# Kernel optimization log

Measured on AMD Instinct MI355X. Metric: run time of the kernel, lower is better.

The kernel has to match this reference:

```python
import jax, jax.numpy as jnp
import numpy as np
import math

B, S, D, H = 2, 2048, 1024, 32
HD = D // H  # head_dim = 32
NEG = -1e9


def setup_inputs() -> dict:
    key = jax.random.key(0)
    ks = jax.random.split(key, 6)
    x = jax.random.normal(ks[0], (B, S, D), dtype=jnp.float32)
    # additive causal mask: 0 on/below diagonal, -1e9 above
    causal = jnp.tril(jnp.ones((S, S), dtype=bool))
    mask = jnp.where(causal, 0.0, NEG).astype(jnp.float32)[None, None]
    # SSMax-style per-query-position log-length scale
    section_log_len = jnp.log(jnp.arange(1, S + 1, dtype=jnp.float32) + 1.0).reshape(1, 1, S, 1)
    sc = 1.0 / math.sqrt(D)
    wq = jax.random.normal(ks[1], (D, D), dtype=jnp.float32) * sc
    wk = jax.random.normal(ks[2], (D, D), dtype=jnp.float32) * sc
    wv = jax.random.normal(ks[3], (D, D), dtype=jnp.float32) * sc
    wo = jax.random.normal(ks[4], (D, D), dtype=jnp.float32) * sc
    seq_scale = jnp.ones((1, H, 1, 1), dtype=jnp.float32)
    return {"x": x, "mask": mask, "section_log_len": section_log_len,
            "wq": wq, "wk": wk, "wv": wv, "wo": wo, "seq_scale": seq_scale}


def reference(x, mask, section_log_len, wq, wk, wv, wo, seq_scale):
    bsz, seqlen, dim = x.shape
    # projections (torch Linear: y = x @ W.T); split heads -> [b, h, s, hd]
    q = (x @ wq.T).reshape(bsz, seqlen, H, HD).transpose(0, 2, 1, 3)
    k = (x @ wk.T).reshape(bsz, seqlen, H, HD).transpose(0, 2, 1, 3)
    v = (x @ wv.T).reshape(bsz, seqlen, H, HD).transpose(0, 2, 1, 3)
    # n_kv_heads == n_heads, so repeat_kv is identity
    scores = jnp.einsum('bhqd,bhkd->bhqk', q, k) / math.sqrt(HD)
    scores = scores * (section_log_len * seq_scale)  # SSMax per-head learned scale
    scores = scores + mask
    probs = jax.nn.softmax(scores.astype(jnp.float32), axis=-1).astype(q.dtype)
    out = jnp.einsum('bhqk,bhkd->bhqd', probs, v)
    out = out.transpose(0, 2, 1, 3).reshape(bsz, seqlen, dim)
    return out @ wo.T
```

## Files before the change

kernel.cpp:

```cpp
#include <hip/hip_runtime.h>
#include <hip/hip_bf16.h>

typedef __bf16 bf16_t;
typedef bf16_t bf16x8 __attribute__((ext_vector_type(8)));
typedef float f32x4 __attribute__((ext_vector_type(4)));

#define NB 2
#define SEQ 2048
#define DIM 1024
#define NH 32
#define HDIM 32

#define LDP 72

static __device__ __forceinline__ f32x4 mfma16(bf16x8 a, bf16x8 b, f32x4 c) {
    return __builtin_amdgcn_mfma_f32_16x16x32_bf16(a, b, c, 0, 0, 0);
}

static __device__ __forceinline__ float fexp2(float x) {
    float r;
    asm("v_exp_f32 %0, %1" : "=v"(r) : "v"(x));
    return r;
}

static __device__ __forceinline__ void load_lds16(const bf16_t* g, bf16_t* l) {
    __builtin_amdgcn_global_load_lds(
        (const __attribute__((address_space(1))) void*)(g),
        (__attribute__((address_space(3))) void*)(l), 16, 0, 0);
}

__global__ __launch_bounds__(256)
void cvt_f32_bf16(const float* __restrict__ s0, bf16_t* __restrict__ d0, int n0,
                  const float* __restrict__ s1, bf16_t* __restrict__ d1, int n1,
                  const float* __restrict__ s2, bf16_t* __restrict__ d2, int n2,
                  const float* __restrict__ s3, bf16_t* __restrict__ d3, int n3,
                  const float* __restrict__ s4, bf16_t* __restrict__ d4, int n4) {
    const int stride = gridDim.x * blockDim.x;
    const int tid = blockIdx.x * blockDim.x + threadIdx.x;
    const float* src[5] = {s0, s1, s2, s3, s4};
    bf16_t* dst[5] = {d0, d1, d2, d3, d4};
    const int n[5] = {n0, n1, n2, n3, n4};
#pragma unroll
    for (int r = 0; r < 5; r++) {
        const int nv = n[r] >> 2;
        for (int i = tid; i < nv; i += stride) {
            float4 v = ((const float4*)src[r])[i];
            bf16_t o[4] = {(bf16_t)v.x, (bf16_t)v.y, (bf16_t)v.z, (bf16_t)v.w};
            *(uint2*)(dst[r] + i * 4) = *(const uint2*)o;
        }
    }
}

template <int EPI, int BM>
__global__ __launch_bounds__(256)
void gemm_pipe(const bf16_t* __restrict__ A, const bf16_t* __restrict__ W,
               float* __restrict__ Cf, bf16_t* __restrict__ qb,
               bf16_t* __restrict__ kb, bf16_t* __restrict__ vtb,
               const float* __restrict__ slen, const float* __restrict__ ss) {
    constexpr int MI = BM / 32;
    constexpr int ABUF = BM * 32;
    __shared__ alignas(16) bf16_t As[3 * ABUF];
    __shared__ alignas(16) bf16_t Bs[3 * 4096];
    const int t = threadIdx.x;
    const int lane = t & 63, wave = t >> 6;
    const int lane16 = lane & 15, quad = lane >> 4;
    const int wm = (wave >> 1) * (BM / 2), wn = (wave & 1) * 64;
    const int id = blockIdx.x;
    int m0, n0g;
    if (EPI == 1) {
        const int xcd = id & 7, slot = id >> 3;
        m0 = (xcd + 8 * (slot & 3)) * 128;
        n0g = (slot >> 2) * 128;
    } else {
        const int xcd = id & 7, slot = id >> 3;
        m0 = (xcd + 8 * (slot & 7)) * 64;
        n0g = (slot >> 3) * 128;
    }
    const int tr = t >> 2;
    const int tc = ((t & 3) ^ ((tr >> 1) & 3)) * 8;
    const bf16_t* ga = A + (m0 + tr) * DIM + tc;
    const bf16_t* gb = W + (n0g + tr) * DIM + tc;
    const int rq = (quad ^ ((lane16 >> 1) & 3)) * 8;
    const bool vseg = (EPI == 1) && (n0g >= 2048);

    f32x4 acc[MI][4];
#pragma unroll
    for (int i = 0; i < MI; i++)
#pragma unroll
        for (int j = 0; j < 4; j++) acc[i][j] = f32x4{0.f, 0.f, 0.f, 0.f};

    auto stage = [&](int k0, int buf) {
        bf16_t* a_dst = As + buf * ABUF + (t & 192) * 8;
        bf16_t* b_dst = Bs + buf * 4096 + (t & 192) * 8;
        load_lds16(ga + k0, a_dst);
        if (BM == 128) load_lds16(ga + 64 * DIM + k0, a_dst + 2048);
        load_lds16(gb + k0, b_dst);
        load_lds16(gb + 64 * DIM + k0, b_dst + 2048);
    };
    auto compute = [&](int buf) {
        bf16x8 af[MI], bfr[4];
#pragma unroll
        for (int mi = 0; mi < MI; mi++)
            af[mi] = *(const bf16x8*)(As + buf * ABUF +
                                      (wm + mi * 16 + lane16) * 32 + rq);
#pragma unroll
        for (int ni = 0; ni < 4; ni++)
            bfr[ni] = *(const bf16x8*)(Bs + buf * 4096 +
                                       (wn + ni * 16 + lane16) * 32 + rq);
        if (vseg) {
#pragma unroll
            for (int mi = 0; mi < MI; mi++)
#pragma unroll
                for (int ni = 0; ni < 4; ni++)
                    acc[mi][ni] = mfma16(bfr[ni], af[mi], acc[mi][ni]);
        } else {
#pragma unroll
            for (int mi = 0; mi < MI; mi++)
#pragma unroll
                for (int ni = 0; ni < 4; ni++)
                    acc[mi][ni] = mfma16(af[mi], bfr[ni], acc[mi][ni]);
        }
    };

    stage(0, 0);
    stage(32, 1);
#pragma unroll
    for (int k0 = 0; k0 < DIM; k0 += 32) {
        const int it = k0 >> 5;
        const int cur = it % 3;
        if (k0 + 64 < DIM) {
            stage(k0 + 64, (it + 2) % 3);
            if (BM == 128)
                asm volatile("s_waitcnt vmcnt(8)" ::: "memory");
            else
                asm volatile("s_waitcnt vmcnt(6)" ::: "memory");
        } else if (k0 + 32 < DIM) {
            if (BM == 128)
                asm volatile("s_waitcnt vmcnt(4)" ::: "memory");
            else
                asm volatile("s_waitcnt vmcnt(3)" ::: "memory");
        } else {
            asm volatile("s_waitcnt vmcnt(0)" ::: "memory");
        }
        asm volatile("s_barrier" ::: "memory");
        compute(cur);
        if (k0 + 32 < DIM) {
            asm volatile("s_waitcnt lgkmcnt(0)" ::: "memory");
            asm volatile("s_barrier" ::: "memory");
        }
    }

    if (EPI == 0) {
#pragma unroll
        for (int mi = 0; mi < MI; mi++)
#pragma unroll
            for (int ni = 0; ni < 4; ni++)
#pragma unroll
                for (int r = 0; r < 4; r++) {
                    int row = m0 + wm + mi * 16 + quad * 4 + r;
                    int col = n0g + wn + ni * 16 + lane16;
                    Cf[row * DIM + col] = acc[mi][ni][r];
                }
    } else if (!vseg) {
        const bool isq = (n0g < 1024);
        bf16_t* dst = isq ? qb : kb;
        const int nb = n0g & 1023;
#pragma unroll
        for (int mi = 0; mi < MI; mi++)
#pragma unroll
            for (int ni = 0; ni < 4; ni++) {
                const int h = ((nb + wn) >> 5) + (ni >> 1);
                const float hscale =
                    isq ? ss[h] * (0.17677669529663687f * 1.4426950408889634f)
                        : 0.f;
#pragma unroll
                for (int r = 0; r < 4; r++) {
                    int m = m0 + wm + mi * 16 + quad * 4 + r;
                    int nl = nb + wn + ni * 16 + lane16;
                    int b = m >> 11, s = m & (SEQ - 1);
                    int d = nl & 31;
                    float v = acc[mi][ni][r];
                    if (isq) v *= slen[s] * hscale;
                    dst[(((b * NH + h) << 11) + s) * 32 + d] = (bf16_t)v;
                }
            }
    } else {
        const int nb = n0g & 1023;
#pragma unroll
        for (int mi = 0; mi < MI; mi++)
#pragma unroll
            for (int ni = 0; ni < 4; ni++)
#pragma unroll
                for (int r = 0; r < 4; r++) {
                    int nl = nb + wn + ni * 16 + quad * 4 + r;
                    int m = m0 + wm + mi * 16 + lane16;
                    int b = m >> 11, s = m & (SEQ - 1);
                    int h = nl >> 5, d = nl & 31;
                    vtb[(((b * NH + h) << 5) + d) * SEQ + s] = (bf16_t)acc[mi][ni][r];
                }
    }
}

__global__ __launch_bounds__(256, 4)
void attn_fwd(const bf16_t* __restrict__ q, const bf16_t* __restrict__ k,
              const bf16_t* __restrict__ vt, bf16_t* __restrict__ out) {
    __shared__ alignas(16) bf16_t pscr[4][2][32 * LDP];
    const int t = threadIdx.x;
    const int lane = t & 63, wave = t >> 6;
    const int lane16 = lane & 15, quad = lane >> 4;
    const int gw = blockIdx.x * 4 + wave;
    const int idx = gw & 63;
    const int qt = (idx & 1) ? (63 - (idx >> 1)) : (idx >> 1);
    const int h = (gw >> 6) & (NH - 1);
    const int b = gw >> 11;
    const int q0 = qt * 32;
    const bf16_t* qh = q + (b * NH + h) * SEQ * HDIM;
    const bf16_t* kh = k + (b * NH + h) * SEQ * HDIM;
    const bf16_t* vth = vt + (b * NH + h) * HDIM * SEQ;

    bf16_t* wb0 = pscr[wave][0] + quad * 4 * LDP + 4 * lane16;
    bf16_t* wb1 = pscr[wave][1] + quad * 4 * LDP + 4 * lane16;
    const bf16_t* rb0 = pscr[wave][0] + lane16 * LDP + quad * 8;
    const bf16_t* rb1 = pscr[wave][1] + lane16 * LDP + quad * 8;

    bf16x8 qf[2];
    qf[0] = *(const bf16x8*)(qh + (q0 + lane16) * HDIM + quad * 8);
    qf[1] = *(const bf16x8*)(qh + (q0 + 16 + lane16) * HDIM + quad * 8);

    bf16x8 ones;
#pragma unroll
    for (int j = 0; j < 8; j++) ones[j] = (bf16_t)1.0f;

    f32x4 o[2][2], ol[2];
#pragma unroll
    for (int mi = 0; mi < 2; mi++) {
        ol[mi] = f32x4{0.f, 0.f, 0.f, 0.f};
#pragma unroll
        for (int ni = 0; ni < 2; ni++) o[mi][ni] = f32x4{0.f, 0.f, 0.f, 0.f};
    }

    const bf16_t* kptr = kh + (4 * lane16) * HDIM + quad * 8;
    const bf16_t* vpa = vth + lane16 * SEQ + quad * 8;
    const bf16_t* vpb = vth + (16 + lane16) * SEQ + quad * 8;

    const f32x4 zz = f32x4{0.f, 0.f, 0.f, 0.f};
    bf16x8 kc[4], vc[4], pf[2][2];

    const int nb64 = (qt >> 1) + 1;

    auto qkexp = [&](int hh, bf16_t* wb, int kv, bool domask) {
        f32x4 sc[2][2];
        __builtin_amdgcn_s_setprio(1);
#pragma unroll
        for (int mi = 0; mi < 2; mi++)
#pragma unroll
            for (int j = 0; j < 2; j++)
                sc[mi][j] = mfma16(qf[mi], kc[2 * hh + j], zz);
        __builtin_amdgcn_s_setprio(0);
#pragma unroll
        for (int mi = 0; mi < 2; mi++)
#pragma unroll
            for (int r = 0; r < 4; r++) {
                float p0 = fexp2(sc[mi][0][r]);
                float p1 = fexp2(sc[mi][1][r]);
                if (domask) {
                    const int rowg = q0 + mi * 16 + quad * 4 + r;
                    if (kv + 4 * lane16 + 2 * hh > rowg) p0 = 0.f;
                    if (kv + 4 * lane16 + 2 * hh + 1 > rowg) p1 = 0.f;
                }
                bf16_t pb[2] = {(bf16_t)p0, (bf16_t)p1};
                *(unsigned int*)(wb + (mi * 16 + r) * LDP + 2 * hh) =
                    *(const unsigned int*)pb;
            }
    };
    auto ldk = [&]() {
#pragma unroll
        for (int tt = 0; tt < 4; tt++) kc[tt] = *(const bf16x8*)(kptr + tt * HDIM);
        kptr += 64 * HDIM;
    };
    auto ldv = [&](int kv) {
        vc[0] = *(const bf16x8*)(vpa + kv);
        vc[1] = *(const bf16x8*)(vpa + kv + 32);
        vc[2] = *(const bf16x8*)(vpb + kv);
        vc[3] = *(const bf16x8*)(vpb + kv + 32);
    };
    auto ldp = [&](const bf16_t* rb) {
#pragma unroll
        for (int mi = 0; mi < 2; mi++) {
            pf[mi][0] = *(const bf16x8*)(rb + mi * 16 * LDP);
            pf[mi][1] = *(const bf16x8*)(rb + mi * 16 * LDP + 32);
        }
    };
    auto pv = [&]() {
        __builtin_amdgcn_s_setprio(1);
#pragma unroll
        for (int mi = 0; mi < 2; mi++) {
#pragma unroll
            for (int ni = 0; ni < 2; ni++) {
                o[mi][ni] = mfma16(pf[mi][0], vc[2 * ni], o[mi][ni]);
                o[mi][ni] = mfma16(pf[mi][1], vc[2 * ni + 1], o[mi][ni]);
            }
            ol[mi] = mfma16(pf[mi][0], ones, ol[mi]);
            ol[mi] = mfma16(pf[mi][1], ones, ol[mi]);
        }
        __builtin_amdgcn_s_setprio(0);
    };

    ldk();
    ldv(0);
    {
        const bool m0only = (nb64 == 1);
        qkexp(0, wb0, 0, m0only);
        bf16x8 ksave[4];
        qkexp(1, wb0, 0, m0only);
        (void)ksave;
        ldk();
    }

    for (int i = 1; i < nb64 - 1; i++) {
        const int kv = i << 6;
        bf16_t* wb = (i & 1) ? wb1 : wb0;
        const bf16_t* rb = (i & 1) ? rb0 : rb1;
        ldp(rb);
        pv();
        ldv(kv);
        qkexp(0, wb, kv, false);
        qkexp(1, wb, kv, false);
        ldk();
    }

    if (nb64 > 1) {
        const int i = nb64 - 1;
        const int kv = i << 6;
        bf16_t* wb = (i & 1) ? wb1 : wb0;
        const bf16_t* rb = (i & 1) ? rb0 : rb1;
        ldp(rb);
        pv();
        ldv(kv);
        qkexp(0, wb, kv, true);
        qkexp(1, wb, kv, true);
    }

    ldp(((nb64 - 1) & 1) ? rb1 : rb0);
    pv();

#pragma unroll
    for (int mi = 0; mi < 2; mi++)
#pragma unroll
        for (int r = 0; r < 4; r++) {
            float inv = 1.0f / ol[mi][r];
            int qi = q0 + mi * 16 + quad * 4 + r;
            bf16_t* ob = out + (b * SEQ + qi) * DIM + h * HDIM;
            ob[lane16] = (bf16_t)(o[mi][0][r] * inv);
            ob[16 + lane16] = (bf16_t)(o[mi][1][r] * inv);
        }
}

extern "C" void kernel_launch(void* const* d_in, const int* in_sizes, int n_in,
                              void* d_out, int out_size, void* d_ws, size_t ws_size,
                              hipStream_t stream) {
    const float* x = (const float*)d_in[0];
    const float* slen = (const float*)d_in[2];
    const float* wq = (const float*)d_in[3];
    const float* wk = (const float*)d_in[4];
    const float* wv = (const float*)d_in[5];
    const float* wo = (const float*)d_in[6];
    const float* ss = (const float*)d_in[7];

    const size_t ELEMS = (size_t)NB * SEQ * DIM;
    const size_t WELEMS = (size_t)DIM * DIM;
    bf16_t* xb = (bf16_t*)d_ws;
    bf16_t* abuf = xb;
    bf16_t* wqkvb = xb + ELEMS;
    bf16_t* wob = wqkvb + 3 * WELEMS;
    bf16_t* qbuf = wob + WELEMS;
    bf16_t* vtbuf = qbuf + ELEMS;
    bf16_t* kbuf = (bf16_t*)d_out;

    dim3 blk(256);
    cvt_f32_bf16<<<dim3(1024), blk, 0, stream>>>(
        x, xb, (int)ELEMS, wq, wqkvb, (int)WELEMS, wk, wqkvb + WELEMS,
        (int)WELEMS, wv, wqkvb + 2 * WELEMS, (int)WELEMS, wo, wob, (int)WELEMS);

    gemm_pipe<1, 128><<<dim3(768), blk, 0, stream>>>(
        xb, wqkvb, nullptr, qbuf, kbuf, vtbuf, slen, ss);
    attn_fwd<<<dim3(NB * NH * (SEQ / 32) / 4), blk, 0, stream>>>(
        qbuf, kbuf, vtbuf, abuf);
    gemm_pipe<0, 64><<<dim3(512), blk, 0, stream>>>(
        abuf, wob, (float*)d_out, nullptr, nullptr, nullptr, nullptr, nullptr);
}
```

Baseline: 210.6 us.

## Balance causal attention by pairing short and long query tiles with split-KV combine

Each block now holds two wave pairs. In each pair, one wave processes a short query tile and then the first part of a long tile's KV range. The other wave processes the rest of that long tile, and partial outputs and row sums are added through LDS before the store. This gives every wave an equal count of 64-wide KV blocks and removes the causal load imbalance. In exchange, the P-scratch double buffering and the K prefetch across iterations are dropped, which adds an LDS combine and a block barrier and may expose more memory latency.

```diff
diff --git a/kernel.cpp b/kernel.cpp
--- a/kernel.cpp
+++ b/kernel.cpp
@@ -204,156 +204,166 @@
 __global__ __launch_bounds__(256, 4)
 void attn_fwd(const bf16_t* __restrict__ q, const bf16_t* __restrict__ k,
               const bf16_t* __restrict__ vt, bf16_t* __restrict__ out) {
-    __shared__ alignas(16) bf16_t pscr[4][2][32 * LDP];
+    __shared__ alignas(16) bf16_t pscr[4][32 * LDP];
+    __shared__ float comb[2][64][25];
     const int t = threadIdx.x;
     const int lane = t & 63, wave = t >> 6;
     const int lane16 = lane & 15, quad = lane >> 4;
-    const int gw = blockIdx.x * 4 + wave;
-    const int idx = gw & 63;
-    const int qt = (idx & 1) ? (63 - (idx >> 1)) : (idx >> 1);
-    const int h = (gw >> 6) & (NH - 1);
-    const int b = gw >> 11;
-    const int q0 = qt * 32;
+    const int bh = blockIdx.x & 63;
+    const int g = blockIdx.x >> 6;
+    const int pairi = wave >> 1;
+    const int role = wave & 1;
+    const int tb = g * 2 + pairi;
+    const int qtA = tb, qtB = 63 - tb;
+    const int naA = (qtA >> 1) + 1;
+    const int nbB = (qtB >> 1) + 1;
+    const int split = 16 - naA;
+    const int h = bh & (NH - 1);
+    const int b = bh >> 5;
     const bf16_t* qh = q + (b * NH + h) * SEQ * HDIM;
     const bf16_t* kh = k + (b * NH + h) * SEQ * HDIM;
     const bf16_t* vth = vt + (b * NH + h) * HDIM * SEQ;
 
-    bf16_t* wb0 = pscr[wave][0] + quad * 4 * LDP + 4 * lane16;
-    bf16_t* wb1 = pscr[wave][1] + quad * 4 * LDP + 4 * lane16;
-    const bf16_t* rb0 = pscr[wave][0] + lane16 * LDP + quad * 8;
-    const bf16_t* rb1 = pscr[wave][1] + lane16 * LDP + quad * 8;
-
-    bf16x8 qf[2];
-    qf[0] = *(const bf16x8*)(qh + (q0 + lane16) * HDIM + quad * 8);
-    qf[1] = *(const bf16x8*)(qh + (q0 + 16 + lane16) * HDIM + quad * 8);
-
-    bf16x8 ones;
-#pragma unroll
-    for (int j = 0; j < 8; j++) ones[j] = (bf16_t)1.0f;
-
-    f32x4 o[2][2], ol[2];
-#pragma unroll
-    for (int mi = 0; mi < 2; mi++) {
-        ol[mi] = f32x4{0.f, 0.f, 0.f, 0.f};
-#pragma unroll
-        for (int ni = 0; ni < 2; ni++) o[mi][ni] = f32x4{0.f, 0.f, 0.f, 0.f};
-    }
-
-    const bf16_t* kptr = kh + (4 * lane16) * HDIM + quad * 8;
+    bf16_t* wb = pscr[wave] + quad * 4 * LDP + 4 * lane16;
+    const bf16_t* rb = pscr[wave] + lane16 * LDP + quad * 8;
+
+    const bf16_t* kp0 = kh + (4 * lane16) * HDIM + quad * 8;
     const bf16_t* vpa = vth + lane16 * SEQ + quad * 8;
     const bf16_t* vpb = vth + (16 + lane16) * SEQ + quad * 8;
 
+    bf16x8 ones;
+#pragma unroll
+    for (int j = 0; j < 8; j++) ones[j] = (bf16_t)1.0f;
+
     const f32x4 zz = f32x4{0.f, 0.f, 0.f, 0.f};
-    bf16x8 kc[4], vc[4], pf[2][2];
-
-    const int nb64 = (qt >> 1) + 1;
-
-    auto qkexp = [&](int hh, bf16_t* wb, int kv, bool domask) {
-        f32x4 sc[2][2];
-        __builtin_amdgcn_s_setprio(1);
+    bf16x8 qf[2];
+    f32x4 o[2][2], ol[2];
+
+    auto zeroacc = [&]() {
+#pragma unroll
+        for (int mi = 0; mi < 2; mi++) {
+            ol[mi] = f32x4{0.f, 0.f, 0.f, 0.f};
+#pragma unroll
+            for (int ni = 0; ni < 2; ni++) o[mi][ni] = f32x4{0.f, 0.f, 0.f, 0.f};
+        }
+    };
+    auto loadQ = [&](int q0) {
+        qf[0] = *(const bf16x8*)(qh + (q0 + lane16) * HDIM + quad * 8);
+        qf[1] = *(const bf16x8*)(qh + (q0 + 16 + lane16) * HDIM + quad * 8);
+    };
+    auto doRange = [&](int q0, int lo, int hi, bool maskLast) {
+        for (int blk = lo; blk < hi; blk++) {
+            const int kv = blk << 6;
+            const bool dm = maskLast && (blk == hi - 1);
+            bf16x8 kc[4], vc[4], pf[2][2];
+            const bf16_t* ks = kp0 + blk * (64 * HDIM);
+#pragma unroll
+            for (int tt = 0; tt < 4; tt++)
+                kc[tt] = *(const bf16x8*)(ks + tt * HDIM);
+            vc[0] = *(const bf16x8*)(vpa + kv);
+            vc[1] = *(const bf16x8*)(vpa + kv + 32);
+            vc[2] = *(const bf16x8*)(vpb + kv);
+            vc[3] = *(const bf16x8*)(vpb + kv + 32);
+#pragma unroll
+            for (int hh = 0; hh < 2; hh++) {
+                f32x4 sc[2][2];
+                __builtin_amdgcn_s_setprio(1);
+#pragma unroll
+                for (int mi = 0; mi < 2; mi++)
+#pragma unroll
+                    for (int j = 0; j < 2; j++)
+                        sc[mi][j] = mfma16(qf[mi], kc[2 * hh + j], zz);
+                __builtin_amdgcn_s_setprio(0);
+#pragma unroll
+                for (int mi = 0; mi < 2; mi++)
+#pragma unroll
+                    for (int r = 0; r < 4; r++) {
+                        float p0 = fexp2(sc[mi][0][r]);
+                        float p1 = fexp2(sc[mi][1][r]);
+                        if (dm) {
+                            const int rowg = q0 + mi * 16 + quad * 4 + r;
+                            if (kv + 4 * lane16 + 2 * hh > rowg) p0 = 0.f;
+                            if (kv + 4 * lane16 + 2 * hh + 1 > rowg) p1 = 0.f;
+                        }
+                        bf16_t pb[2] = {(bf16_t)p0, (bf16_t)p1};
+                        *(unsigned int*)(wb + (mi * 16 + r) * LDP + 2 * hh) =
+                            *(const unsigned int*)pb;
+                    }
+            }
+            asm volatile("s_waitcnt lgkmcnt(0)" ::: "memory");
+#pragma unroll
+            for (int mi = 0; mi < 2; mi++) {
+                pf[mi][0] = *(const bf16x8*)(rb + mi * 16 * LDP);
+                pf[mi][1] = *(const bf16x8*)(rb + mi * 16 * LDP + 32);
+            }
+            __builtin_amdgcn_s_setprio(1);
+#pragma unroll
+            for (int mi = 0; mi < 2; mi++) {
+#pragma unroll
+                for (int ni = 0; ni < 2; ni++) {
+                    o[mi][ni] = mfma16(pf[mi][0], vc[2 * ni], o[mi][ni]);
+                    o[mi][ni] = mfma16(pf[mi][1], vc[2 * ni + 1], o[mi][ni]);
+                }
+                ol[mi] = mfma16(pf[mi][0], ones, ol[mi]);
+                ol[mi] = mfma16(pf[mi][1], ones, ol[mi]);
+            }
+            __builtin_amdgcn_s_setprio(0);
+        }
+    };
+    auto storeTile = [&](int q0) {
 #pragma unroll
         for (int mi = 0; mi < 2; mi++)
 #pragma unroll
-            for (int j = 0; j < 2; j++)
-                sc[mi][j] = mfma16(qf[mi], kc[2 * hh + j], zz);
-        __builtin_amdgcn_s_setprio(0);
+            for (int r = 0; r < 4; r++) {
+                float inv = 1.0f / ol[mi][r];
+                int qi = q0 + mi * 16 + quad * 4 + r;
+                bf16_t* ob = out + (b * SEQ + qi) * DIM + h * HDIM;
+                ob[lane16] = (bf16_t)(o[mi][0][r] * inv);
+                ob[16 + lane16] = (bf16_t)(o[mi][1][r] * inv);
+            }
+    };
+
+    if (role == 0) {
+        zeroacc();
+        loadQ(qtA * 32);
+        doRange(qtA * 32, 0, naA, true);
+        storeTile(qtA * 32);
+        zeroacc();
+        loadQ(qtB * 32);
+        doRange(qtB * 32, 0, split, false);
+        float* cl = &comb[pairi][lane][0];
 #pragma unroll
         for (int mi = 0; mi < 2; mi++)
 #pragma unroll
-            for (int r = 0; r < 4; r++) {
-                float p0 = fexp2(sc[mi][0][r]);
-                float p1 = fexp2(sc[mi][1][r]);
-                if (domask) {
-                    const int rowg = q0 + mi * 16 + quad * 4 + r;
-                    if (kv + 4 * lane16 + 2 * hh > rowg) p0 = 0.f;
-                    if (kv + 4 * lane16 + 2 * hh + 1 > rowg) p1 = 0.f;
-                }
-                bf16_t pb[2] = {(bf16_t)p0, (bf16_t)p1};
-                *(unsigned int*)(wb + (mi * 16 + r) * LDP + 2 * hh) =
-                    *(const unsigned int*)pb;
-            }
-    };
-    auto ldk = [&]() {
-#pragma unroll
-        for (int tt = 0; tt < 4; tt++) kc[tt] = *(const bf16x8*)(kptr + tt * HDIM);
-        kptr += 64 * HDIM;
-    };
-    auto ldv = [&](int kv) {
-        vc[0] = *(const bf16x8*)(vpa + kv);
-        vc[1] = *(const bf16x8*)(vpa + kv + 32);
-        vc[2] = *(const bf16x8*)(vpb + kv);
-        vc[3] = *(const bf16x8*)(vpb + kv + 32);
-    };
-    auto ldp = [&](const bf16_t* rb) {
-#pragma unroll
-        for (int mi = 0; mi < 2; mi++) {
-            pf[mi][0] = *(const bf16x8*)(rb + mi * 16 * LDP);
-            pf[mi][1] = *(const bf16x8*)(rb + mi * 16 * LDP + 32);
-        }
-    };
-    auto pv = [&]() {
-        __builtin_amdgcn_s_setprio(1);
-#pragma unroll
-        for (int mi = 0; mi < 2; mi++) {
-#pragma unroll
-            for (int ni = 0; ni < 2; ni++) {
-                o[mi][ni] = mfma16(pf[mi][0], vc[2 * ni], o[mi][ni]);
-                o[mi][ni] = mfma16(pf[mi][1], vc[2 * ni + 1], o[mi][ni]);
-            }
-            ol[mi] = mfma16(pf[mi][0], ones, ol[mi]);
-            ol[mi] = mfma16(pf[mi][1], ones, ol[mi]);
-        }
-        __builtin_amdgcn_s_setprio(0);
-    };
-
-    ldk();
-    ldv(0);
-    {
-        const bool m0only = (nb64 == 1);
-        qkexp(0, wb0, 0, m0only);
-        bf16x8 ksave[4];
-        qkexp(1, wb0, 0, m0only);
-        (void)ksave;
-        ldk();
-    }
-
-    for (int i = 1; i < nb64 - 1; i++) {
-        const int kv = i << 6;
-        bf16_t* wb = (i & 1) ? wb1 : wb0;
-        const bf16_t* rb = (i & 1) ? rb0 : rb1;
-        ldp(rb);
-        pv();
-        ldv(kv);
-        qkexp(0, wb, kv, false);
-        qkexp(1, wb, kv, false);
-        ldk();
-    }
-
-    if (nb64 > 1) {
-        const int i = nb64 - 1;
-        const int kv = i << 6;
-        bf16_t* wb = (i & 1) ? wb1 : wb0;
-        const bf16_t* rb = (i & 1) ? rb0 : rb1;
-        ldp(rb);
-        pv();
-        ldv(kv);
-        qkexp(0, wb, kv, true);
-        qkexp(1, wb, kv, true);
-    }
-
-    ldp(((nb64 - 1) & 1) ? rb1 : rb0);
-    pv();
-
-#pragma unroll
-    for (int mi = 0; mi < 2; mi++)
-#pragma unroll
-        for (int r = 0; r < 4; r++) {
-            float inv = 1.0f / ol[mi][r];
-            int qi = q0 + mi * 16 + quad * 4 + r;
-            bf16_t* ob = out + (b * SEQ + qi) * DIM + h * HDIM;
-            ob[lane16] = (bf16_t)(o[mi][0][r] * inv);
-            ob[16 + lane16] = (bf16_t)(o[mi][1][r] * inv);
-        }
+            for (int ni = 0; ni < 2; ni++)
+#pragma unroll
+                for (int r = 0; r < 4; r++)
+                    cl[(mi * 2 + ni) * 4 + r] = o[mi][ni][r];
+#pragma unroll
+        for (int mi = 0; mi < 2; mi++)
+#pragma unroll
+            for (int r = 0; r < 4; r++) cl[16 + mi * 4 + r] = ol[mi][r];
+    } else {
+        zeroacc();
+        loadQ(qtB * 32);
+        doRange(qtB * 32, split, nbB, true);
+    }
+    __syncthreads();
+    if (role == 1) {
+        const float* cl = &comb[pairi][lane][0];
+#pragma unroll
+        for (int mi = 0; mi < 2; mi++)
+#pragma unroll
+            for (int ni = 0; ni < 2; ni++)
+#pragma unroll
+                for (int r = 0; r < 4; r++)
+                    o[mi][ni][r] += cl[(mi * 2 + ni) * 4 + r];
+#pragma unroll
+        for (int mi = 0; mi < 2; mi++)
+#pragma unroll
+            for (int r = 0; r < 4; r++) ol[mi][r] += cl[16 + mi * 4 + r];
+        storeTile(qtB * 32);
+    }
 }
 
 extern "C" void kernel_launch(void* const* d_in, const int* in_sizes, int n_in,
```

New measurement: 213.1 us. No clear change (+1.2%).
